# Kernel optimization log

Measured on AMD Instinct MI355X. Metric: run time of the kernel, lower is better.

## Reference

```python
import jax, jax.numpy as jnp
import numpy as np

B, N, IN_DIM, HEADS, PER_HEAD = 8, 512, 256, 4, 32
OUT_DIM = HEADS * PER_HEAD  # 128
NEG_SLOPE = 0.2


def setup_inputs() -> dict:
    key = jax.random.key(0)
    ks = jax.random.split(key, 8)
    x = jax.random.normal(ks[0], (B, N, IN_DIM), jnp.float32)
    adj = jax.random.randint(ks[1], (B, N, N), 0, 2, jnp.int32)
    sl = 1.0 / np.sqrt(IN_DIM)
    W_l = jax.random.normal(ks[2], (IN_DIM, OUT_DIM), jnp.float32) * sl  # source proj
    b_l = jnp.zeros((OUT_DIM,), jnp.float32)
    W_r = jax.random.normal(ks[3], (IN_DIM, OUT_DIM), jnp.float32) * sl  # target proj
    b_r = jnp.zeros((OUT_DIM,), jnp.float32)
    att = jax.random.normal(ks[4], (HEADS, PER_HEAD), jnp.float32) * (1.0 / np.sqrt(PER_HEAD))
    bias = jnp.zeros((OUT_DIM,), jnp.float32)
    return {"x": x, "adj": adj, "W_l": W_l, "b_l": b_l, "W_r": W_r, "b_r": b_r,
            "att": att, "bias": bias}


def _gatv2_single(x_b, adj_b, W_l, b_l, W_r, b_r, att, bias):
    # PyG GATv2Conv: remove_self_loops + add_self_loops -> diagonal forced to 1
    n = x_b.shape[0]
    adj_sl = jnp.fill_diagonal(adj_b, 1, inplace=False)
    # edge_index = adj.nonzero().t(): source = row, target = col
    m = (adj_sl != 0).T  # m[i, j]: source j feeds target i
    xl = (x_b @ W_l + b_l).reshape(n, HEADS, PER_HEAD)  # source-side features
    xr = (x_b @ W_r + b_r).reshape(n, HEADS, PER_HEAD)  # target-side features
    s = xr[:, None] + xl[None, :]                       # [i, j, H, C]
    s = jnp.where(s > 0, s, NEG_SLOPE * s)              # LeakyReLU(0.2)
    e = jnp.einsum('ijhc,hc->ijh', s, att)              # attention logits
    e = jnp.where(m[..., None], e, -jnp.inf)
    alpha = jax.nn.softmax(e, axis=1)                   # softmax over sources j
    out = jnp.einsum('ijh,jhc->ihc', alpha, xl).reshape(n, HEADS * PER_HEAD)
    return out + bias


def reference(x, adj, W_l, b_l, W_r, b_r, att, bias):
    # Sequential per-batch processing, faithful to the original Python loop
    # and keeping the [N,N,H,C] intermediate to one graph at a time.
    def one(args):
        x_b, adj_b = args
        return _gatv2_single(x_b, adj_b, W_l, b_l, W_r, b_r, att, bias)
    return jax.lax.map(one, (x, adj))  # [B, N, OUT_DIM]
```

## Files before the change

kernel.cpp:

```cpp
#include <hip/hip_runtime.h>
#include <hip/hip_bf16.h>

#define B_   8
#define N_   512
#define IND  256
#define H_   4
#define PH   32
#define OD   128
#define TI   4

typedef float v2f __attribute__((ext_vector_type(2)));

#define ATT_SCALE 0.5770780163555854f
#define DLR_SCALE 0.8656170245333781f

template <int PAT>
__device__ __forceinline__ float dpp_add(float x) {
    int yi = __builtin_amdgcn_mov_dpp(__float_as_int(x), PAT, 0xF, 0xF, true);
    return x + __int_as_float(yi);
}

__device__ __forceinline__ float fast_exp2(float x) {
#if __has_builtin(__builtin_amdgcn_exp2f)
    return __builtin_amdgcn_exp2f(x);
#else
    return exp2f(x);
#endif
}

__device__ __forceinline__ void pk_fma(v2f& d, v2f a, v2f b) {
    asm("v_pk_fma_f32 %0, %1, %2, %0" : "+v"(d) : "v"(a), "v"(b));
}
__device__ __forceinline__ v2f pk_add(v2f a, v2f b) {
    v2f d;
    asm("v_pk_add_f32 %0, %1, %2" : "=v"(d) : "v"(a), "v"(b));
    return d;
}

__global__ __launch_bounds__(256, 2) void proj_kernel(
    const float* __restrict__ x,
    const float* __restrict__ Wl, const float* __restrict__ bl,
    const float* __restrict__ Wr, const float* __restrict__ br,
    const float* __restrict__ att,
    float* __restrict__ xl, float* __restrict__ xr,
    float* __restrict__ dl, float* __restrict__ dr)
{
    __shared__ float xs[8 * IND];
    const int t = threadIdx.x;
    const int row0 = blockIdx.x * 8;

    const float4* xp4 = (const float4*)(x + (size_t)row0 * IND);
    float4* xs4 = (float4*)xs;
    #pragma unroll
    for (int k = 0; k < 2; ++k)
        xs4[t + k * 256] = xp4[t + k * 256];
    __syncthreads();

    const int which = t >> 7;
    const int rg = (t >> 6) & 1;
    const int og = t & 63;
    const int o0 = og * 2;
    const int r0 = rg * 4;
    const float* W  = which ? Wr : Wl;
    const float* bb = which ? br : bl;

    float acc0[4], acc1[4];
    #pragma unroll
    for (int r = 0; r < 4; ++r) { acc0[r] = 0.f; acc1[r] = 0.f; }

    for (int k = 0; k < IND; k += 4) {
        float wf0[4], wf1[4];
        #pragma unroll
        for (int kk = 0; kk < 4; ++kk) {
            float2 wv = *(const float2*)(W + (size_t)(k + kk) * OD + o0);
            wf0[kk] = wv.x;
            wf1[kk] = wv.y;
        }
        float xv[4][4];
        #pragma unroll
        for (int r = 0; r < 4; ++r)
            *(float4*)(xv[r]) = *(const float4*)(&xs[(r0 + r) * IND + k]);
        #pragma unroll
        for (int kk = 0; kk < 4; ++kk)
            #pragma unroll
            for (int r = 0; r < 4; ++r) {
                acc0[r] = fmaf(xv[r][kk], wf0[kk], acc0[r]);
                acc1[r] = fmaf(xv[r][kk], wf1[kk], acc1[r]);
            }
    }

    const float bv0 = bb[o0];
    const float bv1 = bb[o0 + 1];
    const float a0 = att[o0];
    const float a1 = att[o0 + 1];
    float* dst = which ? xr : xl;
    float* dp  = which ? dr : dl;
    float dcon[4];
    #pragma unroll
    for (int r = 0; r < 4; ++r) {
        float y0 = acc0[r] + bv0;
        float y1 = acc1[r] + bv1;
        *(float2*)(&dst[(size_t)(row0 + r0 + r) * OD + o0]) = make_float2(y0, y1);
        dcon[r] = fmaf(a0, y0, a1 * y1);
    }
    #pragma unroll
    for (int m = 1; m < 16; m <<= 1) {
        #pragma unroll
        for (int r = 0; r < 4; ++r)
            dcon[r] += __shfl_xor(dcon[r], m);
    }
    if ((og & 15) == 0) {
        const int h = og >> 4;
        #pragma unroll
        for (int r = 0; r < 4; ++r)
            dp[(size_t)(row0 + r0 + r) * H_ + h] = DLR_SCALE * dcon[r];
    }
}

__global__ __launch_bounds__(256, 3) void attn_kernel(
    const int* __restrict__ adj, const float* __restrict__ att,
    const float* __restrict__ bias,
    const float* __restrict__ xl, const float* __restrict__ xr,
    const float* __restrict__ dl, const float* __restrict__ dr,
    float* __restrict__ out)
{
    const int t = threadIdx.x;
    const int b  = blockIdx.x >> 7;
    const int i0 = (blockIdx.x & 127) * TI;
    const int cq = t & 3;
    const int js = (t >> 2) & 15;
    const int h  = t >> 6;
    const int cbase = h * PH + cq * 8;

    float atS[8];
    {
        const float* ap = att + cbase;
        float4 a0 = *(const float4*)(ap);
        float4 a1 = *(const float4*)(ap + 4);
        atS[0] = ATT_SCALE * a0.x; atS[1] = ATT_SCALE * a0.y;
        atS[2] = ATT_SCALE * a0.z; atS[3] = ATT_SCALE * a0.w;
        atS[4] = ATT_SCALE * a1.x; atS[5] = ATT_SCALE * a1.y;
        atS[6] = ATT_SCALE * a1.z; atS[7] = ATT_SCALE * a1.w;
    }
    v2f xr2[TI][4];
    float drv[TI];
    #pragma unroll
    for (int il = 0; il < TI; ++il) {
        const float* xp = xr + ((size_t)(b * N_ + i0 + il)) * OD + cbase;
        float4 r0 = *(const float4*)(xp);
        float4 r1 = *(const float4*)(xp + 4);
        xr2[il][0] = (v2f){r0.x, r0.y};
        xr2[il][1] = (v2f){r0.z, r0.w};
        xr2[il][2] = (v2f){r1.x, r1.y};
        xr2[il][3] = (v2f){r1.z, r1.w};
        drv[il] = dr[((size_t)(b * N_ + i0 + il)) * H_ + h];
    }

    v2f acc[TI][4];
    float sumw[TI];
    #pragma unroll
    for (int il = 0; il < TI; ++il) {
        sumw[il] = 0.f;
        #pragma unroll
        for (int m = 0; m < 4; ++m) acc[il][m] = (v2f){0.f, 0.f};
    }

    const float* xlp = xl + ((size_t)(b * N_ + js)) * OD + cbase;
    const int*   ajp = adj + ((size_t)(b * N_ + js)) * N_ + i0;
    const float* dlp = dl + ((size_t)(b * N_ + js)) * H_ + h;

    float4 va = *(const float4*)(xlp);
    float4 vb = *(const float4*)(xlp + 4);
    int4   mj = *(const int4*)(ajp);
    float  dj = *dlp;

    #pragma unroll 2
    for (int u = 0; u < 32; ++u) {
        float4 wa = va, wb = vb;
        int4   wm = mj;
        float  wd = dj;
        if (u < 31) {
            xlp += 16 * OD; ajp += 16 * N_; dlp += 16 * H_;
            va = *(const float4*)(xlp);
            vb = *(const float4*)(xlp + 4);
            mj = *(const int4*)(ajp);
            dj = *dlp;
        }
        const int j = u * 16 + js;
        v2f p0 = (v2f){wa.x, wa.y}, p1 = (v2f){wa.z, wa.w};
        v2f p2 = (v2f){wb.x, wb.y}, p3 = (v2f){wb.z, wb.w};
        int wmv[TI] = {wm.x, wm.y, wm.z, wm.w};
        #pragma unroll
        for (int il = 0; il < TI; ++il) {
            float e2a = 0.f, e2b = 0.f;
            v2f s;
            s = pk_add(xr2[il][0], p0);
            e2a = fmaf(atS[0], __builtin_fabsf(s.x), e2a);
            e2b = fmaf(atS[1], __builtin_fabsf(s.y), e2b);
            s = pk_add(xr2[il][1], p1);
            e2a = fmaf(atS[2], __builtin_fabsf(s.x), e2a);
            e2b = fmaf(atS[3], __builtin_fabsf(s.y), e2b);
            s = pk_add(xr2[il][2], p2);
            e2a = fmaf(atS[4], __builtin_fabsf(s.x), e2a);
            e2b = fmaf(atS[5], __builtin_fabsf(s.y), e2b);
            s = pk_add(xr2[il][3], p3);
            e2a = fmaf(atS[6], __builtin_fabsf(s.x), e2a);
            e2b = fmaf(atS[7], __builtin_fabsf(s.y), e2b);
            float eh = e2a + e2b;
            eh = dpp_add<0xB1>(eh);
            eh = dpp_add<0x4E>(eh);
            float e = (wd + drv[il]) + eh;
            bool keep = (wmv[il] != 0) || (j == i0 + il);
            float w = keep ? fast_exp2(e) : 0.f;
            sumw[il] += w;
            v2f ws = (v2f){w, w};
            pk_fma(acc[il][0], ws, p0);
            pk_fma(acc[il][1], ws, p1);
            pk_fma(acc[il][2], ws, p2);
            pk_fma(acc[il][3], ws, p3);
        }
    }

    #pragma unroll
    for (int il = 0; il < TI; ++il) {
        sumw[il] += __shfl_xor(sumw[il], 4);
        sumw[il] += __shfl_xor(sumw[il], 8);
        sumw[il] += __shfl_xor(sumw[il], 16);
        sumw[il] += __shfl_xor(sumw[il], 32);
    }

    float accf[32];
    #pragma unroll
    for (int il = 0; il < TI; ++il)
        #pragma unroll
        for (int m = 0; m < 4; ++m) {
            accf[il * 8 + 2 * m]     = acc[il][m].x;
            accf[il * 8 + 2 * m + 1] = acc[il][m].y;
        }

    float r16[16];
    {
        const bool hi = (js & 1) != 0;
        #pragma unroll
        for (int m = 0; m < 16; ++m) {
            float send = hi ? accf[m] : accf[16 + m];
            float keep = hi ? accf[16 + m] : accf[m];
            r16[m] = keep + __shfl_xor(send, 4);
        }
    }
    float r8[8];
    {
        const bool hi = (js & 2) != 0;
        #pragma unroll
        for (int m = 0; m < 8; ++m) {
            float send = hi ? r16[m] : r16[8 + m];
            float keep = hi ? r16[8 + m] : r16[m];
            r8[m] = keep + __shfl_xor(send, 8);
        }
    }
    float r4[4];
    {
        const bool hi = (js & 4) != 0;
        #pragma unroll
        for (int m = 0; m < 4; ++m) {
            float send = hi ? r8[m] : r8[4 + m];
            float keep = hi ? r8[4 + m] : r8[m];
            r4[m] = keep + __shfl_xor(send, 16);
        }
    }
    float r2[2];
    {
        const bool hi = (js & 8) != 0;
        #pragma unroll
        for (int m = 0; m < 2; ++m) {
            float send = hi ? r4[m] : r4[2 + m];
            float keep = hi ? r4[2 + m] : r4[m];
            r2[m] = keep + __shfl_xor(send, 32);
        }
    }

    const int il = ((js & 1) << 1) | ((js >> 1) & 1);
    const int coff = ((js >> 2) & 1) * 4 + ((js >> 3) & 1) * 2;
    const int c = cbase + coff;
    const float sw0 = (js & 1) ? ((js & 2) ? sumw[3] : sumw[2])
                               : ((js & 2) ? sumw[1] : sumw[0]);
    const float inv = 1.f / sw0;
    float* op = out + ((size_t)(b * N_ + i0 + il)) * OD;
    *(float2*)(&op[c]) = make_float2(fmaf(r2[0], inv, bias[c]),
                                     fmaf(r2[1], inv, bias[c + 1]));
}

extern "C" void kernel_launch(void* const* d_in, const int* in_sizes, int n_in,
                              void* d_out, int out_size, void* d_ws, size_t ws_size,
                              hipStream_t stream) {
    const float* x    = (const float*)d_in[0];
    const int*   adj  = (const int*)d_in[1];
    const float* Wl   = (const float*)d_in[2];
    const float* bl   = (const float*)d_in[3];
    const float* Wr   = (const float*)d_in[4];
    const float* br   = (const float*)d_in[5];
    const float* att  = (const float*)d_in[6];
    const float* bias = (const float*)d_in[7];
    float* out = (float*)d_out;

    float* xl = (float*)d_ws;
    float* xr = xl + (size_t)B_ * N_ * OD;
    float* dl = xr + (size_t)B_ * N_ * OD;
    float* dr = dl + (size_t)B_ * N_ * H_;

    proj_kernel<<<512, 256, 0, stream>>>(x, Wl, bl, Wr, br, att, xl, xr, dl, dr);
    attn_kernel<<<1024, 256, 0, stream>>>(adj, att, bias, xl, xr, dl, dr, out);
}
```

Baseline: 122.9 us.

## Pack adjacency into bitmasks in a prepass and read bits in attention

```diff
diff --git a/kernel.cpp b/kernel.cpp
--- a/kernel.cpp
+++ b/kernel.cpp
@@ -35,6 +35,23 @@
     v2f d;
     asm("v_pk_add_f32 %0, %1, %2" : "=v"(d) : "v"(a), "v"(b));
     return d;
+}
+
+__global__ __launch_bounds__(256) void pack_kernel(
+    const int* __restrict__ adj, unsigned long long* __restrict__ pack)
+{
+    const int t = threadIdx.x;
+    const int lane = t & 63;
+    const int r = blockIdx.x * 4 + (t >> 6);
+    const int j = r & (N_ - 1);
+    const int* row = adj + (size_t)r * N_;
+    #pragma unroll
+    for (int k = 0; k < 8; ++k) {
+        const int i = k * 64 + lane;
+        int a = row[i];
+        unsigned long long m = __ballot(a != 0 || i == j);
+        if (lane == 0) pack[(size_t)r * 8 + k] = m;
+    }
 }
 
 __global__ __launch_bounds__(256, 2) void proj_kernel(
@@ -118,7 +135,7 @@
 }
 
 __global__ __launch_bounds__(256, 3) void attn_kernel(
-    const int* __restrict__ adj, const float* __restrict__ att,
+    const unsigned* __restrict__ pack, const float* __restrict__ att,
     const float* __restrict__ bias,
     const float* __restrict__ xl, const float* __restrict__ xr,
     const float* __restrict__ dl, const float* __restrict__ dr,
@@ -131,6 +148,7 @@
     const int js = (t >> 2) & 15;
     const int h  = t >> 6;
     const int cbase = h * PH + cq * 8;
+    const int shift = i0 & 31;
 
     float atS[8];
     {
@@ -165,31 +183,30 @@
         for (int m = 0; m < 4; ++m) acc[il][m] = (v2f){0.f, 0.f};
     }
 
-    const float* xlp = xl + ((size_t)(b * N_ + js)) * OD + cbase;
-    const int*   ajp = adj + ((size_t)(b * N_ + js)) * N_ + i0;
-    const float* dlp = dl + ((size_t)(b * N_ + js)) * H_ + h;
-
-    float4 va = *(const float4*)(xlp);
-    float4 vb = *(const float4*)(xlp + 4);
-    int4   mj = *(const int4*)(ajp);
-    float  dj = *dlp;
+    const float*    xlp = xl + ((size_t)(b * N_ + js)) * OD + cbase;
+    const unsigned* pp  = pack + ((size_t)(b * N_ + js)) * 16 + (i0 >> 5);
+    const float*    dlp = dl + ((size_t)(b * N_ + js)) * H_ + h;
+
+    float4   va = *(const float4*)(xlp);
+    float4   vb = *(const float4*)(xlp + 4);
+    unsigned pj = *pp;
+    float    dj = *dlp;
 
     #pragma unroll 2
     for (int u = 0; u < 32; ++u) {
-        float4 wa = va, wb = vb;
-        int4   wm = mj;
-        float  wd = dj;
+        float4   wa = va, wb = vb;
+        unsigned wp = pj;
+        float    wd = dj;
         if (u < 31) {
-            xlp += 16 * OD; ajp += 16 * N_; dlp += 16 * H_;
+            xlp += 16 * OD; pp += 16 * 16; dlp += 16 * H_;
             va = *(const float4*)(xlp);
             vb = *(const float4*)(xlp + 4);
-            mj = *(const int4*)(ajp);
+            pj = *pp;
             dj = *dlp;
         }
-        const int j = u * 16 + js;
+        const unsigned pbs = wp >> shift;
         v2f p0 = (v2f){wa.x, wa.y}, p1 = (v2f){wa.z, wa.w};
         v2f p2 = (v2f){wb.x, wb.y}, p3 = (v2f){wb.z, wb.w};
-        int wmv[TI] = {wm.x, wm.y, wm.z, wm.w};
         #pragma unroll
         for (int il = 0; il < TI; ++il) {
             float e2a = 0.f, e2b = 0.f;
@@ -210,8 +227,8 @@
             eh = dpp_add<0xB1>(eh);
             eh = dpp_add<0x4E>(eh);
             float e = (wd + drv[il]) + eh;
-            bool keep = (wmv[il] != 0) || (j == i0 + il);
-            float w = keep ? fast_exp2(e) : 0.f;
+            float ex = fast_exp2(e);
+            float w = (pbs & (1u << il)) ? ex : 0.f;
             sumw[il] += w;
             v2f ws = (v2f){w, w};
             pk_fma(acc[il][0], ws, p0);
@@ -307,7 +324,11 @@
     float* xr = xl + (size_t)B_ * N_ * OD;
     float* dl = xr + (size_t)B_ * N_ * OD;
     float* dr = dl + (size_t)B_ * N_ * H_;
-
+    unsigned long long* pack =
+        (unsigned long long*)(dr + (size_t)B_ * N_ * H_);
+
+    pack_kernel<<<1024, 256, 0, stream>>>(adj, pack);
     proj_kernel<<<512, 256, 0, stream>>>(x, Wl, bl, Wr, br, att, xl, xr, dl, dr);
-    attn_kernel<<<1024, 256, 0, stream>>>(adj, att, bias, xl, xr, dl, dr, out);
-}
+    attn_kernel<<<1024, 256, 0, stream>>>((const unsigned*)pack, att, bias,
+                                          xl, xr, dl, dr, out);
+}
```

After: 126.0 us. 2.5% more time.
